# Performance work log

Hardware: AMD Instinct MI355X
Metric: run time of the kernel (lower is better)

The kernel has to match this reference:

```python
import jax, jax.numpy as jnp
import numpy as np

ALPHA = 0.2  # LeakyReLU negative slope

def setup_inputs() -> dict:
    key = jax.random.key(0)
    k1, k2, k3 = jax.random.split(key, 3)
    B, N, Fin, Fout = 8, 2048, 256, 128
    h = jax.random.normal(k1, (B, N, Fin), dtype=jnp.float32)
    W = jax.random.normal(k2, (Fin, Fout), dtype=jnp.float32) * (1.414 / np.sqrt(Fin))
    a = jax.random.normal(k3, (2 * Fout, 1), dtype=jnp.float32) * 0.1
    return {"h": h, "W": W, "a": a}

def reference(h, W, a):
    # Wh: [B, N, D]
    Wh = jnp.einsum('bni,io->bno', h, W)
    D = Wh.shape[-1]
    a1 = a[:D, 0]   # weights for the 'i' (repeat_interleave) half
    a2 = a[D:, 0]   # weights for the 'j' (repeat) half
    s1 = Wh @ a1    # [B, N]
    s2 = Wh @ a2    # [B, N]
    # e[b,i,j] = leakyrelu(s1[b,i] + s2[b,j])  (fused form of the O(N^2*2D) concat)
    e = s1[:, :, None] + s2[:, None, :]
    e = jnp.where(e >= 0, e, ALPHA * e)
    # original applies softmax over dim=1 (the i axis)
    attention = jax.nn.softmax(e, axis=1)
    # dropout is identity in eval mode
    h_prime = jnp.einsum('bij,bjd->bid', attention, Wh)
    # concat=True -> ELU
    return jax.nn.elu(h_prime)
```

## Files before the change

kernel.cpp:

```cpp
#include <hip/hip_runtime.h>
#include <hip/hip_bf16.h>


#define ALPHA 0.2f
#define LOG2E 1.4426950408889634f
constexpr int Bb=8, Nn=2048, FIN=256, FOUT=128;

typedef __attribute__((ext_vector_type(8))) short short8;
typedef __attribute__((ext_vector_type(4))) float f32x4;
typedef __attribute__((ext_vector_type(16))) float f32x16;
typedef const __attribute__((address_space(1))) unsigned int* gptr_t;
typedef __attribute__((address_space(3))) unsigned int* lptr_t;

__device__ __forceinline__ float lrelu(float x){ return fmaxf(x, ALPHA*x); }
__device__ __forceinline__ unsigned short bfbits(float x){
    __hip_bfloat16 h = __float2bfloat16(x);
    return *(unsigned short*)&h;
}

__global__ __launch_bounds__(256) void k_prep(const float* __restrict__ W,
                                              __hip_bfloat16* __restrict__ WTt){
    const int idx = blockIdx.x*256 + threadIdx.x;
    #pragma unroll
    for (int v = 0; v < 4; ++v){
        const int widx = idx + v*8192;
        const int kk = widx & 31, n = (widx>>5)&127, kt = widx>>12;
        WTt[widx] = __float2bfloat16(W[(kt*32+kk)*FOUT + n]);
    }
}

__global__ __launch_bounds__(256) void k_wh(const float* __restrict__ h,
                                            const float* __restrict__ a,
                                            const __hip_bfloat16* __restrict__ WTt,
                                            float* __restrict__ s1,
                                            float* __restrict__ s2,
                                            __hip_bfloat16* __restrict__ WhT){
    const int blk = blockIdx.x;
    const int rowbase = blk * 32;
    const int b = blk >> 6;
    const int jt = (rowbase & (Nn-1)) >> 5;
    const int t = threadIdx.x;
    const int wave = t>>6, lane = t&63;
    const int wm = wave & 1, wn = wave >> 1;
    const int lm = lane & 15, q = lane >> 4;

    __shared__ __align__(16) float hs[32*260];
    __shared__ unsigned short tt[FOUT*40];
    __shared__ float s1red[2][32], s2red[2][32];

    {
        const float* srcbase = h + (size_t)rowbase*FIN;
        #pragma unroll
        for (int c = 0; c < 8; ++c){
            const int row = wave*8 + c;
            __builtin_amdgcn_global_load_lds(
                (gptr_t)(srcbase + (size_t)row*FIN + lane*4),
                (lptr_t)&hs[row*260], 16, 0, 0);
        }
    }
    __syncthreads();

    f32x4 acc[4];
    #pragma unroll
    for (int ntl = 0; ntl < 4; ++ntl) acc[ntl] = (f32x4){0.f,0.f,0.f,0.f};

    const float* hrow = &hs[(wm*16 + lm)*260];
    const short* Wt = (const short*)WTt;
    #pragma unroll
    for (int kt = 0; kt < 8; ++kt){
        float av[8];
        *(float4*)&av[0] = *(const float4*)&hrow[kt*32 + q*8];
        *(float4*)&av[4] = *(const float4*)&hrow[kt*32 + q*8 + 4];
        short8 afr;
        #pragma unroll
        for (int e = 0; e < 8; ++e) afr[e] = (short)bfbits(av[e]);
        #pragma unroll
        for (int ntl = 0; ntl < 4; ++ntl){
            const short8 bfr = *(const short8*)(Wt + ((kt*128 + wn*64 + ntl*16 + lm)*32 + q*8));
            acc[ntl] = __builtin_amdgcn_mfma_f32_16x16x32_bf16(afr, bfr, acc[ntl], 0,0,0);
        }
    }

    {
        float a1v[4], a2v[4];
        #pragma unroll
        for (int ntl = 0; ntl < 4; ++ntl){
            a1v[ntl] = a[wn*64 + ntl*16 + lm];
            a2v[ntl] = a[FOUT + wn*64 + ntl*16 + lm];
        }
        #pragma unroll
        for (int rg = 0; rg < 4; ++rg){
            float p1 = 0.f, p2 = 0.f;
            #pragma unroll
            for (int ntl = 0; ntl < 4; ++ntl){
                p1 += acc[ntl][rg]*a1v[ntl];
                p2 += acc[ntl][rg]*a2v[ntl];
            }
            #pragma unroll
            for (int m = 1; m < 16; m <<= 1){
                p1 += __shfl_xor(p1, m);
                p2 += __shfl_xor(p2, m);
            }
            if (lm == 0){
                s1red[wn][wm*16 + q*4 + rg] = p1;
                s2red[wn][wm*16 + q*4 + rg] = p2;
            }
        }
    }

    #pragma unroll
    for (int ntl = 0; ntl < 4; ++ntl){
        ushort4 u;
        u.x = bfbits(acc[ntl][0]); u.y = bfbits(acc[ntl][1]);
        u.z = bfbits(acc[ntl][2]); u.w = bfbits(acc[ntl][3]);
        *(ushort4*)&tt[(wn*64 + ntl*16 + lm)*40 + wm*16 + q*4] = u;
    }
    __syncthreads();

    if (t < 32){
        s1[rowbase + t] = (s1red[0][t] + s1red[1][t]) * LOG2E;
        s2[rowbase + t] = (s2red[0][t] + s2red[1][t]) * LOG2E;
    }
    {
        const int d = t >> 1, jsub16 = t & 1;
        const unsigned short* src = &tt[d*40 + jsub16*16];
        short8 v0 = *(const short8*)src;
        short8 v1 = *(const short8*)(src + 8);
        const int s  = (jt & 1)*2 + jsub16;
        const int nt = d >> 5, col = d & 31;
        const int u0 = (s*4 + nt)*64 + col;
        short* Wo = (short*)WhT;
        const size_t tb = ((size_t)(b*32 + (jt >> 1)))*8192;
        *(short8*)&Wo[tb + (size_t)u0*8]      = v0;
        *(short8*)&Wo[tb + (size_t)(u0+32)*8] = v1;
    }
}

__global__ __launch_bounds__(256) void k_z(const float* __restrict__ s1,
                                           const float* __restrict__ s2,
                                           float* __restrict__ l2z){
    const int b  = blockIdx.x >> 6;
    const int jt = blockIdx.x & 63;
    const int t  = threadIdx.x;
    const int jj = t & 31, part = t >> 5;
    const int j  = jt*32 + jj;
    __shared__ float s1s[Nn];
    __shared__ float red[8][33];

    {
        const float4* g = (const float4*)(s1 + (size_t)b*Nn);
        float4* p = (float4*)s1s;
        #pragma unroll
        for (int v0 = 0; v0 < 2; ++v0){ const int v = t + v0*256; p[v] = g[v]; }
    }
    __syncthreads();
    const float s2j = s2[b*Nn + j];
    float sum = 0.f;
    const float4* s4 = (const float4*)&s1s[part*256];
    #pragma unroll 4
    for (int v = 0; v < 64; ++v){
        float x[4]; *(float4*)x = s4[v];
        sum += __builtin_amdgcn_exp2f(lrelu(x[0]+s2j))
             + __builtin_amdgcn_exp2f(lrelu(x[1]+s2j))
             + __builtin_amdgcn_exp2f(lrelu(x[2]+s2j))
             + __builtin_amdgcn_exp2f(lrelu(x[3]+s2j));
    }
    red[part][jj] = sum;
    __syncthreads();
    if (part == 0){
        float Z = 0.f;
        #pragma unroll
        for (int p = 0; p < 8; ++p) Z += red[p][jj];
        l2z[b*Nn + j] = -__builtin_amdgcn_logf(Z);
    }
}

__global__ __launch_bounds__(512, 2) void k_pv(const float* __restrict__ s1,
                                               const float* __restrict__ s2,
                                               const float* __restrict__ l2z,
                                               const __hip_bfloat16* __restrict__ WhT,
                                               float* __restrict__ out){
    const int blk   = blockIdx.x;
    const int b     = blk & 7;
    const int ibase = (blk >> 3) * 64;
    const int t     = threadIdx.x;
    const int wave  = t >> 6, lane = t & 63;
    const int wr = wave & 1, kh = wave >> 1;
    const int il = lane & 31, l5 = lane >> 5;

    __shared__ float s2s[Nn], lzs[Nn];
    __shared__ unsigned short Bs[2][4][8192];

    {
        const float4* g1 = (const float4*)(s2  + (size_t)b*Nn);
        const float4* g2 = (const float4*)(l2z + (size_t)b*Nn);
        ((float4*)s2s)[t] = g1[t];
        ((float4*)lzs)[t] = g2[t];
    }

    const float s1a = s1[(size_t)b*Nn + ibase + wr*32 + il];

    f32x16 acc[4];
    #pragma unroll
    for (int nt = 0; nt < 4; ++nt)
        #pragma unroll
        for (int e = 0; e < 16; ++e) acc[nt][e] = 0.f;

    const char* Wtb = (const char*)WhT + (size_t)b*32*16384;
    const int laneoff = wr*8192 + lane*16;

    {
        const char* src = Wtb + (size_t)(kh*8)*16384 + laneoff;
        unsigned short* dst = &Bs[0][kh][wr*4096];
        #pragma unroll
        for (int c = 0; c < 8; ++c)
            __builtin_amdgcn_global_load_lds((gptr_t)(src + c*1024),
                                             (lptr_t)(dst + c*512), 16, 0, 0);
    }

    int buf = 0;
    for (int it = 0; it < 8; ++it){
        __syncthreads();
        if (it + 1 < 8){
            const char* src = Wtb + (size_t)(kh*8 + it + 1)*16384 + laneoff;
            unsigned short* dst = &Bs[buf^1][kh][wr*4096];
            #pragma unroll
            for (int c = 0; c < 8; ++c)
                __builtin_amdgcn_global_load_lds((gptr_t)(src + c*1024),
                                                 (lptr_t)(dst + c*512), 16, 0, 0);
        }
        const char* tile = (const char*)&Bs[buf][kh][0];
        #pragma unroll
        for (int s = 0; s < 4; ++s){
            short8 bfr[4];
            #pragma unroll
            for (int nt = 0; nt < 4; ++nt)
                bfr[nt] = *(const short8*)(tile + ((s*4 + nt)*64 + lane)*16);

            const int jb = kh*512 + it*64 + s*16 + l5*8;
            float sarr[8], larr[8];
            *(float4*)&sarr[0] = *(const float4*)&s2s[jb];
            *(float4*)&sarr[4] = *(const float4*)&s2s[jb+4];
            *(float4*)&larr[0] = *(const float4*)&lzs[jb];
            *(float4*)&larr[4] = *(const float4*)&lzs[jb+4];
            short8 afa;
            #pragma unroll
            for (int e = 0; e < 8; ++e){
                const float z = s1a + sarr[e];
                afa[e] = (short)bfbits(__builtin_amdgcn_exp2f(fmaxf(z, ALPHA*z) + larr[e]));
            }
            #pragma unroll
            for (int nt = 0; nt < 4; ++nt)
                acc[nt] = __builtin_amdgcn_mfma_f32_32x32x16_bf16(afa, bfr[nt], acc[nt], 0,0,0);
        }
        buf ^= 1;
    }

    __syncthreads();
    float* comb = (float*)&Bs[0][0][0];
    if (kh < 2){
        float* cb = comb + (size_t)(kh*2 + wr)*(32*132);
        #pragma unroll
        for (int nt = 0; nt < 4; ++nt)
            #pragma unroll
            for (int r = 0; r < 16; ++r){
                const int row = (r&3) + 8*(r>>2) + 4*l5;
                cb[row*132 + nt*32 + il] = acc[nt][r];
            }
    }
    __syncthreads();
    if (kh >= 2){
        float* cb = comb + (size_t)((kh-2)*2 + wr)*(32*132);
        #pragma unroll
        for (int nt = 0; nt < 4; ++nt)
            #pragma unroll
            for (int r = 0; r < 16; ++r){
                const int row = (r&3) + 8*(r>>2) + 4*l5;
                cb[row*132 + nt*32 + il] += acc[nt][r];
            }
    }
    __syncthreads();
    {
        const int rgrp = t >> 5, c4 = (t & 31)*4;
        #pragma unroll
        for (int rr = 0; rr < 4; ++rr){
            const int row = rgrp*4 + rr;
            const int wrr = row >> 5, rin = row & 31;
            const float* r0 = comb + (size_t)(wrr)*(32*132)       + rin*132 + c4;
            const float* r1 = comb + (size_t)(2 + wrr)*(32*132)   + rin*132 + c4;
            float4 v0 = *(const float4*)r0, v1 = *(const float4*)r1;
            float o[4];
            #pragma unroll
            for (int e = 0; e < 4; ++e){
                const float x = ((const float*)&v0)[e] + ((const float*)&v1)[e];
                o[e] = x > 0.f ? x : expm1f(x);
            }
            *(float4*)&out[((size_t)(b*Nn + ibase + row))*FOUT + c4] = *(float4*)o;
        }
    }
}

extern "C" void kernel_launch(void* const* d_in, const int* in_sizes, int n_in,
                              void* d_out, int out_size, void* d_ws, size_t ws_size,
                              hipStream_t stream) {
    (void)in_sizes; (void)n_in; (void)out_size; (void)ws_size;
    const float* h = (const float*)d_in[0];
    const float* W = (const float*)d_in[1];
    const float* a = (const float*)d_in[2];
    float* out = (float*)d_out;

    float* ws    = (float*)d_ws;
    float* s1    = ws;
    float* s2    = s1 + Bb*Nn;
    float* l2z   = s2 + Bb*Nn;
    __hip_bfloat16* WTt = (__hip_bfloat16*)(l2z + Bb*Nn);
    __hip_bfloat16* WhT = WTt + 32768;

    k_prep<<<dim3(32),        dim3(256), 0, stream>>>(W, WTt);
    k_wh  <<<dim3(Bb*Nn/32),  dim3(256), 0, stream>>>(h, a, WTt, s1, s2, WhT);
    k_z   <<<dim3(Bb*64),     dim3(256), 0, stream>>>(s1, s2, l2z);
    k_pv  <<<dim3(Bb*Nn/64),  dim3(512), 0, stream>>>(s1, s2, l2z, WhT, out);
}
```

Baseline: 100.1 us.

## Fold leaky-ReLU and log-normalizer into per-column arrays; read B operand directly from global

k_z now writes two per-column arrays, s2+lz and alpha*s2+lz, so k_pv computes each attention weight as exp2(max(s1+A, alpha*s1+B)), using the identity that a positive scale commutes with max. k_pv drops the LDS staging of s2/lz and the double-buffered global_load_lds pipeline for WhT tiles, and loads MFMA B fragments and the column arrays straight from global/L2. This removes the LDS traffic and per-iteration block barriers, and the smaller LDS footprint plus the relaxed launch bound may change occupancy. The cost is that MFMA issue now waits on global-memory latency without explicit prefetch.

```diff
diff --git a/kernel.cpp b/kernel.cpp
--- a/kernel.cpp
+++ b/kernel.cpp
@@ -138,7 +138,8 @@
 
 __global__ __launch_bounds__(256) void k_z(const float* __restrict__ s1,
                                            const float* __restrict__ s2,
-                                           float* __restrict__ l2z){
+                                           float* __restrict__ Aout,
+                                           float* __restrict__ Bout){
     const int b  = blockIdx.x >> 6;
     const int jt = blockIdx.x & 63;
     const int t  = threadIdx.x;
@@ -171,15 +172,17 @@
         float Z = 0.f;
         #pragma unroll
         for (int p = 0; p < 8; ++p) Z += red[p][jj];
-        l2z[b*Nn + j] = -__builtin_amdgcn_logf(Z);
-    }
-}
-
-__global__ __launch_bounds__(512, 2) void k_pv(const float* __restrict__ s1,
-                                               const float* __restrict__ s2,
-                                               const float* __restrict__ l2z,
-                                               const __hip_bfloat16* __restrict__ WhT,
-                                               float* __restrict__ out){
+        const float lz = -__builtin_amdgcn_logf(Z);
+        Aout[b*Nn + j] = s2j + lz;
+        Bout[b*Nn + j] = ALPHA*s2j + lz;
+    }
+}
+
+__global__ __launch_bounds__(512) void k_pv(const float* __restrict__ s1,
+                                            const float* __restrict__ Aarr,
+                                            const float* __restrict__ Barr,
+                                            const __hip_bfloat16* __restrict__ WhT,
+                                            float* __restrict__ out){
     const int blk   = blockIdx.x;
     const int b     = blk & 7;
     const int ibase = (blk >> 3) * 64;
@@ -188,17 +191,12 @@
     const int wr = wave & 1, kh = wave >> 1;
     const int il = lane & 31, l5 = lane >> 5;
 
-    __shared__ float s2s[Nn], lzs[Nn];
-    __shared__ unsigned short Bs[2][4][8192];
-
-    {
-        const float4* g1 = (const float4*)(s2  + (size_t)b*Nn);
-        const float4* g2 = (const float4*)(l2z + (size_t)b*Nn);
-        ((float4*)s2s)[t] = g1[t];
-        ((float4*)lzs)[t] = g2[t];
-    }
-
-    const float s1a = s1[(size_t)b*Nn + ibase + wr*32 + il];
+    __shared__ __align__(16) float comb[4*32*132];
+
+    const float s1a  = s1[(size_t)b*Nn + ibase + wr*32 + il];
+    const float as1a = ALPHA * s1a;
+    const float* Ab = Aarr + (size_t)b*Nn;
+    const float* Zb = Barr + (size_t)b*Nn;
 
     f32x16 acc[4];
     #pragma unroll
@@ -207,57 +205,34 @@
         for (int e = 0; e < 16; ++e) acc[nt][e] = 0.f;
 
     const char* Wtb = (const char*)WhT + (size_t)b*32*16384;
-    const int laneoff = wr*8192 + lane*16;
-
-    {
-        const char* src = Wtb + (size_t)(kh*8)*16384 + laneoff;
-        unsigned short* dst = &Bs[0][kh][wr*4096];
-        #pragma unroll
-        for (int c = 0; c < 8; ++c)
-            __builtin_amdgcn_global_load_lds((gptr_t)(src + c*1024),
-                                             (lptr_t)(dst + c*512), 16, 0, 0);
-    }
-
-    int buf = 0;
+
     for (int it = 0; it < 8; ++it){
-        __syncthreads();
-        if (it + 1 < 8){
-            const char* src = Wtb + (size_t)(kh*8 + it + 1)*16384 + laneoff;
-            unsigned short* dst = &Bs[buf^1][kh][wr*4096];
-            #pragma unroll
-            for (int c = 0; c < 8; ++c)
-                __builtin_amdgcn_global_load_lds((gptr_t)(src + c*1024),
-                                                 (lptr_t)(dst + c*512), 16, 0, 0);
-        }
-        const char* tile = (const char*)&Bs[buf][kh][0];
+        const char* tile = Wtb + (size_t)(kh*8 + it)*16384;
         #pragma unroll
         for (int s = 0; s < 4; ++s){
             short8 bfr[4];
             #pragma unroll
             for (int nt = 0; nt < 4; ++nt)
-                bfr[nt] = *(const short8*)(tile + ((s*4 + nt)*64 + lane)*16);
+                bfr[nt] = *(const short8*)(tile + (size_t)(((s*4 + nt)*64 + lane)*16));
 
             const int jb = kh*512 + it*64 + s*16 + l5*8;
-            float sarr[8], larr[8];
-            *(float4*)&sarr[0] = *(const float4*)&s2s[jb];
-            *(float4*)&sarr[4] = *(const float4*)&s2s[jb+4];
-            *(float4*)&larr[0] = *(const float4*)&lzs[jb];
-            *(float4*)&larr[4] = *(const float4*)&lzs[jb+4];
+            float av[8], bv[8];
+            *(float4*)&av[0] = *(const float4*)&Ab[jb];
+            *(float4*)&av[4] = *(const float4*)&Ab[jb+4];
+            *(float4*)&bv[0] = *(const float4*)&Zb[jb];
+            *(float4*)&bv[4] = *(const float4*)&Zb[jb+4];
             short8 afa;
             #pragma unroll
-            for (int e = 0; e < 8; ++e){
-                const float z = s1a + sarr[e];
-                afa[e] = (short)bfbits(__builtin_amdgcn_exp2f(fmaxf(z, ALPHA*z) + larr[e]));
-            }
+            for (int e = 0; e < 8; ++e)
+                afa[e] = (short)bfbits(__builtin_amdgcn_exp2f(
+                             fmaxf(s1a + av[e], as1a + bv[e])));
             #pragma unroll
             for (int nt = 0; nt < 4; ++nt)
                 acc[nt] = __builtin_amdgcn_mfma_f32_32x32x16_bf16(afa, bfr[nt], acc[nt], 0,0,0);
         }
-        buf ^= 1;
-    }
-
-    __syncthreads();
-    float* comb = (float*)&Bs[0][0][0];
+    }
+
+    __syncthreads();
     if (kh < 2){
         float* cb = comb + (size_t)(kh*2 + wr)*(32*132);
         #pragma unroll
@@ -312,12 +287,13 @@
     float* ws    = (float*)d_ws;
     float* s1    = ws;
     float* s2    = s1 + Bb*Nn;
-    float* l2z   = s2 + Bb*Nn;
-    __hip_bfloat16* WTt = (__hip_bfloat16*)(l2z + Bb*Nn);
+    float* Aarr  = s2 + Bb*Nn;
+    float* Barr  = Aarr + Bb*Nn;
+    __hip_bfloat16* WTt = (__hip_bfloat16*)(Barr + Bb*Nn);
     __hip_bfloat16* WhT = WTt + 32768;
 
     k_prep<<<dim3(32),        dim3(256), 0, stream>>>(W, WTt);
     k_wh  <<<dim3(Bb*Nn/32),  dim3(256), 0, stream>>>(h, a, WTt, s1, s2, WhT);
-    k_z   <<<dim3(Bb*64),     dim3(256), 0, stream>>>(s1, s2, l2z);
-    k_pv  <<<dim3(Bb*Nn/64),  dim3(512), 0, stream>>>(s1, s2, l2z, WhT, out);
-}
+    k_z   <<<dim3(Bb*64),     dim3(256), 0, stream>>>(s1, s2, Aarr, Barr);
+    k_pv  <<<dim3(Bb*Nn/64),  dim3(512), 0, stream>>>(s1, Aarr, Barr, WhT, out);
+}
```

Result: slower. 103.5 us (+3.5%).
